# Performance work log

Hardware: AMD Instinct MI355X
Metric: run time of the kernel (lower is better)

## Reference

```python
import jax, jax.numpy as jnp
import numpy as np

T, B, I, H = 512, 64, 512, 512


def setup_inputs() -> dict:
    key = jax.random.key(0)
    k1, k2 = jax.random.split(key)
    x = jax.random.normal(k1, (T, B, I), dtype=jnp.float32)
    hidden_state = jnp.zeros((1, B, H), dtype=jnp.float32)
    cell_state = jnp.zeros((1, B, H), dtype=jnp.float32)
    # xavier-uniform-like init for weights, zeros for bias (matches init_weights)
    limit = float(np.sqrt(6.0 / ((I + H) + 4 * H)))
    W = jax.random.uniform(k2, (I + H, 4 * H), minval=-limit, maxval=limit, dtype=jnp.float32)
    b = jnp.zeros((4 * H,), dtype=jnp.float32)
    return {"x": x, "hidden_state": hidden_state, "cell_state": cell_state, "W": W, "b": b}


def reference(x, hidden_state, cell_state, W, b):
    # x: [T,B,I]; states: [1,B,H] -> squeeze leading dim for the scan carry
    h0 = hidden_state[0]
    c0 = cell_state[0]

    def step(carry, x_t):
        h, c = carry
        gates = jnp.concatenate([x_t, h], axis=-1) @ W + b  # [B,4H]
        f = jax.nn.sigmoid(gates[:, :H])
        i = jax.nn.sigmoid(gates[:, H:2 * H])
        cand = jnp.tanh(gates[:, 2 * H:3 * H])
        o = jax.nn.sigmoid(gates[:, 3 * H:])
        c_new = f * c + i * cand
        h_new = o * jnp.tanh(c_new)
        return (h_new, c_new), h_new

    (h_T, c_T), output = jax.lax.scan(step, (h0, c0), x)
    # hidden/cell states returned as [layers, B, H] with layers=1
    return output, (h_T[None], c_T[None])
```

## Files before the change

### kernel.cpp

```cpp
#include <hip/hip_runtime.h>
#include <cstdint>
#include <cstddef>

typedef unsigned short u16;
typedef unsigned long long u64;
typedef __attribute__((ext_vector_type(4))) float f32x4;
typedef __attribute__((ext_vector_type(8))) short s16x8;

#define T_STEPS 512
#define OUT_MAIN 16777216
#define HSLOT 65536

static __device__ __forceinline__ u16 f2bf(float f) {
  unsigned u = __builtin_bit_cast(unsigned, f);
  unsigned r = u + 0x7FFFu + ((u >> 16) & 1u);
  return (u16)(r >> 16);
}
static __device__ __forceinline__ float bf2f(u16 h) {
  unsigned u = ((unsigned)h) << 16;
  return __builtin_bit_cast(float, u);
}

__global__ void init_k(const float* __restrict__ W, const float* __restrict__ h0,
                       const float* __restrict__ c0,
                       u16* __restrict__ wthi, u16* __restrict__ wtlo,
                       u16* __restrict__ hbhi, u16* __restrict__ hblo,
                       float* __restrict__ cws, unsigned* __restrict__ flags) {
  const int NW = 1024 * 2048;
  const int NH = 64 * 512;
  const int total = NW + 2 * NH + 256;
  for (int idx = blockIdx.x * blockDim.x + threadIdx.x; idx < total;
       idx += gridDim.x * blockDim.x) {
    if (idx < NW) {
      int k = idx >> 11;
      int c = idx & 2047;
      float wv = W[idx];
      u16 hi = f2bf(wv);
      wthi[(size_t)c * 1024 + k] = hi;
      wtlo[(size_t)c * 1024 + k] = f2bf(wv - bf2f(hi));
    } else if (idx < NW + NH) {
      int r = idx - NW; int b = r >> 9; int k = r & 511;
      int g = b >> 3, rr = b & 7;
      float v = h0[r];
      u16 hi = f2bf(v);
      int pos = (g * 16 + rr) * 512 + k;
      hbhi[pos] = hi;
      hblo[pos] = f2bf(v - bf2f(hi));
    } else if (idx < NW + 2 * NH) {
      int r = idx - NW - NH;
      cws[r] = c0[r];
    } else {
      flags[idx - NW - 2 * NH] = 0u;
    }
  }
}

__global__ void convx_k(const float* __restrict__ x, u16* __restrict__ hi,
                        u16* __restrict__ lo, int n4) {
  for (int i = blockIdx.x * blockDim.x + threadIdx.x; i < n4;
       i += gridDim.x * blockDim.x) {
    float4 v = ((const float4*)x)[i];
    ushort4 h, l2;
    h.x = f2bf(v.x); l2.x = f2bf(v.x - bf2f(h.x));
    h.y = f2bf(v.y); l2.y = f2bf(v.y - bf2f(h.y));
    h.z = f2bf(v.z); l2.z = f2bf(v.z - bf2f(h.z));
    h.w = f2bf(v.w); l2.w = f2bf(v.w - bf2f(h.w));
    ((ushort4*)hi)[i] = h;
    ((ushort4*)lo)[i] = l2;
  }
}

__global__ void __launch_bounds__(256, 2)
gemm_k(const u16* __restrict__ xhi, const u16* __restrict__ xlo,
       const u16* __restrict__ wthi, const u16* __restrict__ wtlo,
       const float* __restrict__ bias, float* __restrict__ Gout) {
  __shared__ u16 Ah[4096], Al[4096], Bh[4096], Bl[4096];
  const int tid = threadIdx.x;
  const int nb = blockIdx.x & 15;
  const int mb = blockIdx.x >> 4;
  const int w = tid >> 6, l = tid & 63;
  const int wm = w >> 1, wn = w & 1;
  const int lr = l & 15, lq = l >> 4;

  const int pos0 = tid, pos1 = tid + 256;
  const int row0 = pos0 >> 2, row1 = pos1 >> 2;
  const int cc = (tid & 3) * 8;
  const size_t aOff0 = (size_t)(mb * 128 + row0) * 512 + cc;
  const size_t aOff1 = (size_t)(mb * 128 + row1) * 512 + cc;
  const size_t bOff0 = (size_t)(nb * 128 + row0) * 1024 + cc;
  const size_t bOff1 = (size_t)(nb * 128 + row1) * 1024 + cc;

  float bv[4];
  #pragma unroll
  for (int n = 0; n < 4; ++n) bv[n] = bias[nb * 128 + wn * 64 + n * 16 + lr];

  f32x4 acc[4][4] = {};
  s16x8 rA0, rA1, rAl0, rAl1, rB0, rB1, rBl0, rBl1;
  rA0  = *(const s16x8*)(xhi  + aOff0);
  rA1  = *(const s16x8*)(xhi  + aOff1);
  rAl0 = *(const s16x8*)(xlo  + aOff0);
  rAl1 = *(const s16x8*)(xlo  + aOff1);
  rB0  = *(const s16x8*)(wthi + bOff0);
  rB1  = *(const s16x8*)(wthi + bOff1);
  rBl0 = *(const s16x8*)(wtlo + bOff0);
  rBl1 = *(const s16x8*)(wtlo + bOff1);

  for (int kt = 0; kt < 16; ++kt) {
    *(s16x8*)&Ah[pos0 * 8] = rA0;  *(s16x8*)&Ah[pos1 * 8] = rA1;
    *(s16x8*)&Al[pos0 * 8] = rAl0; *(s16x8*)&Al[pos1 * 8] = rAl1;
    *(s16x8*)&Bh[pos0 * 8] = rB0;  *(s16x8*)&Bh[pos1 * 8] = rB1;
    *(s16x8*)&Bl[pos0 * 8] = rBl0; *(s16x8*)&Bl[pos1 * 8] = rBl1;
    __syncthreads();
    if (kt < 15) {
      const int k0 = (kt + 1) * 32;
      rA0  = *(const s16x8*)(xhi  + aOff0 + k0);
      rA1  = *(const s16x8*)(xhi  + aOff1 + k0);
      rAl0 = *(const s16x8*)(xlo  + aOff0 + k0);
      rAl1 = *(const s16x8*)(xlo  + aOff1 + k0);
      rB0  = *(const s16x8*)(wthi + bOff0 + k0);
      rB1  = *(const s16x8*)(wthi + bOff1 + k0);
      rBl0 = *(const s16x8*)(wtlo + bOff0 + k0);
      rBl1 = *(const s16x8*)(wtlo + bOff1 + k0);
    }
    s16x8 fAh[4], fAl[4], fBh[4], fBl[4];
    #pragma unroll
    for (int mm = 0; mm < 4; ++mm) {
      const int rrow = wm * 64 + mm * 16 + lr;
      fAh[mm] = *(const s16x8*)&Ah[rrow * 32 + lq * 8];
      fAl[mm] = *(const s16x8*)&Al[rrow * 32 + lq * 8];
    }
    #pragma unroll
    for (int nn = 0; nn < 4; ++nn) {
      const int crow = wn * 64 + nn * 16 + lr;
      fBh[nn] = *(const s16x8*)&Bh[crow * 32 + lq * 8];
      fBl[nn] = *(const s16x8*)&Bl[crow * 32 + lq * 8];
    }
    #pragma unroll
    for (int mm = 0; mm < 4; ++mm)
      #pragma unroll
      for (int nn = 0; nn < 4; ++nn) {
        acc[mm][nn] = __builtin_amdgcn_mfma_f32_16x16x32_bf16(fAh[mm], fBh[nn], acc[mm][nn], 0, 0, 0);
        acc[mm][nn] = __builtin_amdgcn_mfma_f32_16x16x32_bf16(fAh[mm], fBl[nn], acc[mm][nn], 0, 0, 0);
        acc[mm][nn] = __builtin_amdgcn_mfma_f32_16x16x32_bf16(fAl[mm], fBh[nn], acc[mm][nn], 0, 0, 0);
      }
    __syncthreads();
  }
  #pragma unroll
  for (int mm = 0; mm < 4; ++mm)
    #pragma unroll
    for (int nn = 0; nn < 4; ++nn)
      #pragma unroll
      for (int i = 0; i < 4; ++i) {
        const int row = mb * 128 + wm * 64 + mm * 16 + lq * 4 + i;
        const int col = nb * 128 + wn * 64 + nn * 16 + lr;
        Gout[(size_t)row * 2048 + col] = acc[mm][nn][i] + bv[nn];
      }
}

__global__ void __launch_bounds__(256, 1)
rec_k(const u16* __restrict__ wthi, const u16* __restrict__ wtlo,
      const float* __restrict__ Gbuf,
      u16* __restrict__ hbhi, u16* __restrict__ hblo,
      float* __restrict__ cws, float* __restrict__ out,
      unsigned* __restrict__ flags, int t0, int Tc) {
  const int g = blockIdx.x & 7;
  const int m = blockIdx.x >> 3;
  const int tid = threadIdx.x;
  const int w = tid >> 6;
  const int l = tid & 63;
  const int lr = l & 15, lq = l >> 4;

  __shared__ float part[4][8][64];

  s16x8 bhi[4][4], blo[4][4];
  #pragma unroll
  for (int nt = 0; nt < 4; ++nt) {
    const size_t cb = (size_t)(nt * 512 + m * 16 + lr) * 1024 + 512 + w * 128 + lq * 8;
    #pragma unroll
    for (int kt = 0; kt < 4; ++kt) {
      bhi[kt][nt] = *(const s16x8*)(wthi + cb + kt * 32);
      blo[kt][nt] = *(const s16x8*)(wtlo + cb + kt * 32);
    }
  }

  const int b0 = l >> 3;
  const int jj = (l & 7) * 2;
  float c0r = 0.f, c1r = 0.f;
  if (w == 0) {
    const float* cp = cws + (size_t)(g * 8 + b0) * 512 + m * 16 + jj;
    c0r = cp[0]; c1r = cp[1];
  }
  unsigned* gf = flags + g * 32;
  const int fragBase = (g * 16 + lr) * 128 + w * 32 + lq * 2;

  for (int tl = 0; tl < Tc; ++tl) {
    const int t = t0 + tl;
    float2 gv0, gv1, gv2, gv3;
    if (w == 0) {
      const float* gp = Gbuf + ((size_t)tl * 64 + g * 8 + b0) * 2048 + m * 16 + jj;
      gv0 = *(const float2*)(gp);
      gv1 = *(const float2*)(gp + 512);
      gv2 = *(const float2*)(gp + 1024);
      gv3 = *(const float2*)(gp + 1536);
      const unsigned tgt = (unsigned)t;
      int ok; unsigned spin = 0;
      do {
        unsigned v = 0xFFFFFFFFu;
        if (l < 32 && l != m)
          v = __hip_atomic_load(&gf[l], __ATOMIC_RELAXED, __HIP_MEMORY_SCOPE_AGENT);
        ok = __all((int)(v >= tgt));
        if (!ok) __builtin_amdgcn_s_sleep(2);
      } while (!ok && ++spin < (1u << 27));
    }
    __syncthreads();

    s16x8 ah[4], al[4];
    if (lr < 8) {
      const u64* sH = (const u64*)hbhi + (size_t)((t & 1) * (HSLOT / 4)) + fragBase;
      const u64* sL = (const u64*)hblo + (size_t)((t & 1) * (HSLOT / 4)) + fragBase;
      #pragma unroll
      for (int kt = 0; kt < 4; ++kt) {
        union { u64 q[2]; s16x8 v; } uh, ul;
        uh.q[0] = __hip_atomic_load((u64*)(sH + kt * 8),     __ATOMIC_RELAXED, __HIP_MEMORY_SCOPE_AGENT);
        uh.q[1] = __hip_atomic_load((u64*)(sH + kt * 8 + 1), __ATOMIC_RELAXED, __HIP_MEMORY_SCOPE_AGENT);
        ul.q[0] = __hip_atomic_load((u64*)(sL + kt * 8),     __ATOMIC_RELAXED, __HIP_MEMORY_SCOPE_AGENT);
        ul.q[1] = __hip_atomic_load((u64*)(sL + kt * 8 + 1), __ATOMIC_RELAXED, __HIP_MEMORY_SCOPE_AGENT);
        ah[kt] = uh.v; al[kt] = ul.v;
      }
    } else {
      #pragma unroll
      for (int kt = 0; kt < 4; ++kt) {
        ah[kt] = (s16x8)(short)0; al[kt] = (s16x8)(short)0;
      }
    }

    f32x4 acc[4] = {};
    #pragma unroll
    for (int kt = 0; kt < 4; ++kt)
      #pragma unroll
      for (int nt = 0; nt < 4; ++nt) {
        acc[nt] = __builtin_amdgcn_mfma_f32_16x16x32_bf16(ah[kt], bhi[kt][nt], acc[nt], 0, 0, 0);
        acc[nt] = __builtin_amdgcn_mfma_f32_16x16x32_bf16(ah[kt], blo[kt][nt], acc[nt], 0, 0, 0);
        acc[nt] = __builtin_amdgcn_mfma_f32_16x16x32_bf16(al[kt], bhi[kt][nt], acc[nt], 0, 0, 0);
      }
    if (l < 32) {
      #pragma unroll
      for (int nt = 0; nt < 4; ++nt)
        #pragma unroll
        for (int i = 0; i < 4; ++i)
          part[w][lq * 4 + i][nt * 16 + lr] = acc[nt][i];
    }
    __syncthreads();

    if (w == 0) {
      float ga[4][2];
      #pragma unroll
      for (int gi = 0; gi < 4; ++gi) {
        float2 s0 = *(const float2*)&part[0][b0][gi * 16 + jj];
        float2 s1 = *(const float2*)&part[1][b0][gi * 16 + jj];
        float2 s2 = *(const float2*)&part[2][b0][gi * 16 + jj];
        float2 s3 = *(const float2*)&part[3][b0][gi * 16 + jj];
        ga[gi][0] = (s0.x + s1.x) + (s2.x + s3.x);
        ga[gi][1] = (s0.y + s1.y) + (s2.y + s3.y);
      }
      float fg0 = ga[0][0] + gv0.x, fg1 = ga[0][1] + gv0.y;
      float ig0 = ga[1][0] + gv1.x, ig1 = ga[1][1] + gv1.y;
      float cg0 = ga[2][0] + gv2.x, cg1 = ga[2][1] + gv2.y;
      float og0 = ga[3][0] + gv3.x, og1 = ga[3][1] + gv3.y;
      float fs0 = 1.f / (1.f + __expf(-fg0)), fs1 = 1.f / (1.f + __expf(-fg1));
      float is0 = 1.f / (1.f + __expf(-ig0)), is1 = 1.f / (1.f + __expf(-ig1));
      float os0 = 1.f / (1.f + __expf(-og0)), os1 = 1.f / (1.f + __expf(-og1));
      float cd0 = tanhf(cg0), cd1 = tanhf(cg1);
      c0r = fs0 * c0r + is0 * cd0;
      c1r = fs1 * c1r + is1 * cd1;
      float hn0 = os0 * tanhf(c0r), hn1 = os1 * tanhf(c1r);
      u16 h0h = f2bf(hn0), h1h = f2bf(hn1);
      u16 l0h = f2bf(hn0 - bf2f(h0h)), l1h = f2bf(hn1 - bf2f(h1h));
      const int pdw = ((t + 1) & 1) * (HSLOT / 2) + (g * 16 + b0) * 256 + (m * 16 + jj) / 2;
      unsigned hw2 = (unsigned)h0h | ((unsigned)h1h << 16);
      unsigned lw2 = (unsigned)l0h | ((unsigned)l1h << 16);
      __hip_atomic_store((unsigned*)hbhi + pdw, hw2, __ATOMIC_RELAXED, __HIP_MEMORY_SCOPE_AGENT);
      __hip_atomic_store((unsigned*)hblo + pdw, lw2, __ATOMIC_RELAXED, __HIP_MEMORY_SCOPE_AGENT);
      asm volatile("s_waitcnt vmcnt(0)" ::: "memory");
      if (l == 0)
        __hip_atomic_store(&gf[m], (unsigned)(t + 1), __ATOMIC_RELAXED, __HIP_MEMORY_SCOPE_AGENT);
      float2 ho; ho.x = hn0; ho.y = hn1;
      *(float2*)(out + ((size_t)t * 64 + g * 8 + b0) * 512 + m * 16 + jj) = ho;
      if (t == T_STEPS - 1) {
        *(float2*)(out + (size_t)OUT_MAIN + (size_t)(g * 8 + b0) * 512 + m * 16 + jj) = ho;
        float2 co; co.x = c0r; co.y = c1r;
        *(float2*)(out + (size_t)OUT_MAIN + 32768 + (size_t)(g * 8 + b0) * 512 + m * 16 + jj) = co;
      }
      if (tl == Tc - 1) {
        float* cp = cws + (size_t)(g * 8 + b0) * 512 + m * 16 + jj;
        cp[0] = c0r; cp[1] = c1r;
      }
    }
  }
}

extern "C" void kernel_launch(void* const* d_in, const int* in_sizes, int n_in,
                              void* d_out, int out_size, void* d_ws, size_t ws_size,
                              hipStream_t stream) {
  const float* x  = (const float*)d_in[0];
  const float* h0 = (const float*)d_in[1];
  const float* c0 = (const float*)d_in[2];
  const float* W  = (const float*)d_in[3];
  const float* bs = (const float*)d_in[4];
  float* out = (float*)d_out;

  auto need = [](int tc) -> size_t {
    size_t s = 0;
    s += (size_t)tc * 524288;
    s += (size_t)tc * 131072;
    s += 2 * (size_t)4194304;
    s += 2 * (size_t)262144;
    s += 131072;
    s += 1024 + 8192;
    return s;
  };
  int Tc = 512;
  while (Tc > 2 && need(Tc) > ws_size) Tc >>= 1;

  char* p = (char*)d_ws;
  auto alloc = [&](size_t bytes) -> char* {
    char* r = p;
    p += (bytes + 255) & ~(size_t)255;
    return r;
  };
  float* Gbuf = (float*)alloc((size_t)Tc * 524288);
  u16* xhi  = (u16*)alloc((size_t)Tc * 65536);
  u16* xlo  = (u16*)alloc((size_t)Tc * 65536);
  u16* wthi = (u16*)alloc(4194304);
  u16* wtlo = (u16*)alloc(4194304);
  u16* hbhi = (u16*)alloc(262144);
  u16* hblo = (u16*)alloc(262144);
  float* cws = (float*)alloc(131072);
  unsigned* flags = (unsigned*)alloc(1024);

  hipLaunchKernelGGL(init_k, dim3(1024), dim3(256), 0, stream,
                     W, h0, c0, wthi, wtlo, hbhi, hblo, cws, flags);
  const int nch = 512 / Tc;
  for (int ck = 0; ck < nch; ++ck) {
    const float* xck = x + (size_t)ck * Tc * 64 * 512;
    int n4 = Tc * 64 * 512 / 4;
    hipLaunchKernelGGL(convx_k, dim3(1024), dim3(256), 0, stream, xck, xhi, xlo, n4);
    hipLaunchKernelGGL(gemm_k, dim3(Tc / 2 * 16), dim3(256), 0, stream,
                       xhi, xlo, wthi, wtlo, bs, Gbuf);
    hipLaunchKernelGGL(rec_k, dim3(256), dim3(256), 0, stream,
                       wthi, wtlo, Gbuf, hbhi, hblo, cws, out, flags, ck * Tc, Tc);
  }
}
```

Measured before the change: 2.272 ms.

## Replace flag-based step barrier with timestamp-tagged hidden state words

Removes the per-group flag array and the wait-for-flags-then-load sequence. Each hidden-state element becomes a 64-bit word that holds the step number alongside the bf16 hi/lo pair, so consumers spin directly on the data they need until every tag matches. This drops one global round trip, the store fence and the block barrier per timestep. It also spreads the gate epilogue over 32 lanes in each of the four waves instead of one wave, double-buffers the shared partial sums, and swaps tanhf for a clamped exp-based tanh. In exchange the hidden buffer doubles in size, each lane polls 32 words per spin, and the tanh approximation shifts numerics slightly.

Result: slower. 2.830 ms (+24.6%).

```diff
diff --git a/kernel.cpp b/kernel.cpp
--- a/kernel.cpp
+++ b/kernel.cpp
@@ -9,7 +9,7 @@
 
 #define T_STEPS 512
 #define OUT_MAIN 16777216
-#define HSLOT 65536
+#define HQSLOT 32768
 
 static __device__ __forceinline__ u16 f2bf(float f) {
   unsigned u = __builtin_bit_cast(unsigned, f);
@@ -24,11 +24,10 @@
 __global__ void init_k(const float* __restrict__ W, const float* __restrict__ h0,
                        const float* __restrict__ c0,
                        u16* __restrict__ wthi, u16* __restrict__ wtlo,
-                       u16* __restrict__ hbhi, u16* __restrict__ hblo,
-                       float* __restrict__ cws, unsigned* __restrict__ flags) {
+                       u64* __restrict__ hq, float* __restrict__ cws) {
   const int NW = 1024 * 2048;
   const int NH = 64 * 512;
-  const int total = NW + 2 * NH + 256;
+  const int total = NW + 2 * NH;
   for (int idx = blockIdx.x * blockDim.x + threadIdx.x; idx < total;
        idx += gridDim.x * blockDim.x) {
     if (idx < NW) {
@@ -39,18 +38,14 @@
       wthi[(size_t)c * 1024 + k] = hi;
       wtlo[(size_t)c * 1024 + k] = f2bf(wv - bf2f(hi));
     } else if (idx < NW + NH) {
-      int r = idx - NW; int b = r >> 9; int k = r & 511;
-      int g = b >> 3, rr = b & 7;
+      int r = idx - NW;
       float v = h0[r];
       u16 hi = f2bf(v);
-      int pos = (g * 16 + rr) * 512 + k;
-      hbhi[pos] = hi;
-      hblo[pos] = f2bf(v - bf2f(hi));
-    } else if (idx < NW + 2 * NH) {
+      u16 lo = f2bf(v - bf2f(hi));
+      hq[r] = ((u64)(unsigned)hi << 16) | (u64)(unsigned)lo;
+    } else {
       int r = idx - NW - NH;
       cws[r] = c0[r];
-    } else {
-      flags[idx - NW - 2 * NH] = 0u;
     }
   }
 }
@@ -159,10 +154,8 @@
 
 __global__ void __launch_bounds__(256, 1)
 rec_k(const u16* __restrict__ wthi, const u16* __restrict__ wtlo,
-      const float* __restrict__ Gbuf,
-      u16* __restrict__ hbhi, u16* __restrict__ hblo,
-      float* __restrict__ cws, float* __restrict__ out,
-      unsigned* __restrict__ flags, int t0, int Tc) {
+      const float* __restrict__ Gbuf, u64* __restrict__ hq,
+      float* __restrict__ cws, float* __restrict__ out, int t0, int Tc) {
   const int g = blockIdx.x & 7;
   const int m = blockIdx.x >> 3;
   const int tid = threadIdx.x;
@@ -170,7 +163,7 @@
   const int l = tid & 63;
   const int lr = l & 15, lq = l >> 4;
 
-  __shared__ float part[4][8][64];
+  __shared__ float part[2][4][8][64];
 
   s16x8 bhi[4][4], blo[4][4];
   #pragma unroll
@@ -183,50 +176,49 @@
     }
   }
 
-  const int b0 = l >> 3;
-  const int jj = (l & 7) * 2;
-  float c0r = 0.f, c1r = 0.f;
-  if (w == 0) {
-    const float* cp = cws + (size_t)(g * 8 + b0) * 512 + m * 16 + jj;
-    c0r = cp[0]; c1r = cp[1];
-  }
-  unsigned* gf = flags + g * 32;
-  const int fragBase = (g * 16 + lr) * 128 + w * 32 + lq * 2;
+  const int eb = 2 * w + (l >> 4);
+  const int eu = l & 15;
+  float cr = 0.f;
+  if (l < 32) cr = cws[(size_t)(g * 8 + eb) * 512 + m * 16 + eu];
+
+  const int rowBase = (g * 8 + lr) * 512 + w * 128 + lq * 8;
 
   for (int tl = 0; tl < Tc; ++tl) {
     const int t = t0 + tl;
-    float2 gv0, gv1, gv2, gv3;
-    if (w == 0) {
-      const float* gp = Gbuf + ((size_t)tl * 64 + g * 8 + b0) * 2048 + m * 16 + jj;
-      gv0 = *(const float2*)(gp);
-      gv1 = *(const float2*)(gp + 512);
-      gv2 = *(const float2*)(gp + 1024);
-      gv3 = *(const float2*)(gp + 1536);
-      const unsigned tgt = (unsigned)t;
-      int ok; unsigned spin = 0;
-      do {
-        unsigned v = 0xFFFFFFFFu;
-        if (l < 32 && l != m)
-          v = __hip_atomic_load(&gf[l], __ATOMIC_RELAXED, __HIP_MEMORY_SCOPE_AGENT);
-        ok = __all((int)(v >= tgt));
-        if (!ok) __builtin_amdgcn_s_sleep(2);
-      } while (!ok && ++spin < (1u << 27));
-    }
-    __syncthreads();
+    float gvf = 0.f, gvi = 0.f, gvc = 0.f, gvo = 0.f;
+    if (l < 32) {
+      const float* gp = Gbuf + ((size_t)tl * 64 + g * 8 + eb) * 2048 + m * 16 + eu;
+      gvf = gp[0]; gvi = gp[512]; gvc = gp[1024]; gvo = gp[1536];
+    }
+    const u64* hp = hq + (size_t)(t & 1) * HQSLOT + rowBase;
+    u64 q[4][8];
+    int ok; unsigned spin = 0;
+    do {
+      unsigned bad = 0;
+      if (lr < 8) {
+        #pragma unroll
+        for (int kt = 0; kt < 4; ++kt)
+          #pragma unroll
+          for (int j = 0; j < 8; ++j) {
+            q[kt][j] = __hip_atomic_load(hp + kt * 32 + j, __ATOMIC_RELAXED,
+                                         __HIP_MEMORY_SCOPE_AGENT);
+            bad |= (unsigned)(q[kt][j] >> 32) ^ (unsigned)t;
+          }
+      }
+      ok = __all(bad == 0);
+      if (!ok) __builtin_amdgcn_s_sleep(1);
+    } while (!ok && ++spin < (1u << 26));
 
     s16x8 ah[4], al[4];
     if (lr < 8) {
-      const u64* sH = (const u64*)hbhi + (size_t)((t & 1) * (HSLOT / 4)) + fragBase;
-      const u64* sL = (const u64*)hblo + (size_t)((t & 1) * (HSLOT / 4)) + fragBase;
-      #pragma unroll
-      for (int kt = 0; kt < 4; ++kt) {
-        union { u64 q[2]; s16x8 v; } uh, ul;
-        uh.q[0] = __hip_atomic_load((u64*)(sH + kt * 8),     __ATOMIC_RELAXED, __HIP_MEMORY_SCOPE_AGENT);
-        uh.q[1] = __hip_atomic_load((u64*)(sH + kt * 8 + 1), __ATOMIC_RELAXED, __HIP_MEMORY_SCOPE_AGENT);
-        ul.q[0] = __hip_atomic_load((u64*)(sL + kt * 8),     __ATOMIC_RELAXED, __HIP_MEMORY_SCOPE_AGENT);
-        ul.q[1] = __hip_atomic_load((u64*)(sL + kt * 8 + 1), __ATOMIC_RELAXED, __HIP_MEMORY_SCOPE_AGENT);
-        ah[kt] = uh.v; al[kt] = ul.v;
-      }
+      #pragma unroll
+      for (int kt = 0; kt < 4; ++kt)
+        #pragma unroll
+        for (int j = 0; j < 8; ++j) {
+          unsigned d = (unsigned)q[kt][j];
+          ah[kt][j] = (short)(d >> 16);
+          al[kt][j] = (short)(d & 0xFFFFu);
+        }
     } else {
       #pragma unroll
       for (int kt = 0; kt < 4; ++kt) {
@@ -243,58 +235,52 @@
         acc[nt] = __builtin_amdgcn_mfma_f32_16x16x32_bf16(ah[kt], blo[kt][nt], acc[nt], 0, 0, 0);
         acc[nt] = __builtin_amdgcn_mfma_f32_16x16x32_bf16(al[kt], bhi[kt][nt], acc[nt], 0, 0, 0);
       }
+    const int p = tl & 1;
     if (l < 32) {
       #pragma unroll
       for (int nt = 0; nt < 4; ++nt)
         #pragma unroll
         for (int i = 0; i < 4; ++i)
-          part[w][lq * 4 + i][nt * 16 + lr] = acc[nt][i];
+          part[p][w][lq * 4 + i][nt * 16 + lr] = acc[nt][i];
     }
     __syncthreads();
 
-    if (w == 0) {
-      float ga[4][2];
+    if (l < 32) {
+      float ga[4];
       #pragma unroll
       for (int gi = 0; gi < 4; ++gi) {
-        float2 s0 = *(const float2*)&part[0][b0][gi * 16 + jj];
-        float2 s1 = *(const float2*)&part[1][b0][gi * 16 + jj];
-        float2 s2 = *(const float2*)&part[2][b0][gi * 16 + jj];
-        float2 s3 = *(const float2*)&part[3][b0][gi * 16 + jj];
-        ga[gi][0] = (s0.x + s1.x) + (s2.x + s3.x);
-        ga[gi][1] = (s0.y + s1.y) + (s2.y + s3.y);
-      }
-      float fg0 = ga[0][0] + gv0.x, fg1 = ga[0][1] + gv0.y;
-      float ig0 = ga[1][0] + gv1.x, ig1 = ga[1][1] + gv1.y;
-      float cg0 = ga[2][0] + gv2.x, cg1 = ga[2][1] + gv2.y;
-      float og0 = ga[3][0] + gv3.x, og1 = ga[3][1] + gv3.y;
-      float fs0 = 1.f / (1.f + __expf(-fg0)), fs1 = 1.f / (1.f + __expf(-fg1));
-      float is0 = 1.f / (1.f + __expf(-ig0)), is1 = 1.f / (1.f + __expf(-ig1));
-      float os0 = 1.f / (1.f + __expf(-og0)), os1 = 1.f / (1.f + __expf(-og1));
-      float cd0 = tanhf(cg0), cd1 = tanhf(cg1);
-      c0r = fs0 * c0r + is0 * cd0;
-      c1r = fs1 * c1r + is1 * cd1;
-      float hn0 = os0 * tanhf(c0r), hn1 = os1 * tanhf(c1r);
-      u16 h0h = f2bf(hn0), h1h = f2bf(hn1);
-      u16 l0h = f2bf(hn0 - bf2f(h0h)), l1h = f2bf(hn1 - bf2f(h1h));
-      const int pdw = ((t + 1) & 1) * (HSLOT / 2) + (g * 16 + b0) * 256 + (m * 16 + jj) / 2;
-      unsigned hw2 = (unsigned)h0h | ((unsigned)h1h << 16);
-      unsigned lw2 = (unsigned)l0h | ((unsigned)l1h << 16);
-      __hip_atomic_store((unsigned*)hbhi + pdw, hw2, __ATOMIC_RELAXED, __HIP_MEMORY_SCOPE_AGENT);
-      __hip_atomic_store((unsigned*)hblo + pdw, lw2, __ATOMIC_RELAXED, __HIP_MEMORY_SCOPE_AGENT);
-      asm volatile("s_waitcnt vmcnt(0)" ::: "memory");
-      if (l == 0)
-        __hip_atomic_store(&gf[m], (unsigned)(t + 1), __ATOMIC_RELAXED, __HIP_MEMORY_SCOPE_AGENT);
-      float2 ho; ho.x = hn0; ho.y = hn1;
-      *(float2*)(out + ((size_t)t * 64 + g * 8 + b0) * 512 + m * 16 + jj) = ho;
+        float s0 = part[p][0][eb][gi * 16 + eu];
+        float s1 = part[p][1][eb][gi * 16 + eu];
+        float s2 = part[p][2][eb][gi * 16 + eu];
+        float s3 = part[p][3][eb][gi * 16 + eu];
+        ga[gi] = (s0 + s1) + (s2 + s3);
+      }
+      float fg = ga[0] + gvf, ig = ga[1] + gvi;
+      float cg = ga[2] + gvc, og = ga[3] + gvo;
+      float fs = 1.f / (1.f + __expf(-fg));
+      float is = 1.f / (1.f + __expf(-ig));
+      float os = 1.f / (1.f + __expf(-og));
+      float cgc = fminf(fmaxf(cg, -15.f), 15.f);
+      float e2c = __expf(2.f * cgc);
+      float cd = (e2c - 1.f) / (e2c + 1.f);
+      cr = fs * cr + is * cd;
+      float crc = fminf(fmaxf(cr, -15.f), 15.f);
+      float e2h = __expf(2.f * crc);
+      float th = (e2h - 1.f) / (e2h + 1.f);
+      float hn = os * th;
+      u16 hh = f2bf(hn);
+      u16 hl = f2bf(hn - bf2f(hh));
+      u64 qv = ((u64)(unsigned)(t + 1) << 32) | ((u64)(unsigned)hh << 16) | (u64)(unsigned)hl;
+      __hip_atomic_store(hq + (size_t)((t + 1) & 1) * HQSLOT +
+                             (size_t)(g * 8 + eb) * 512 + m * 16 + eu,
+                         qv, __ATOMIC_RELAXED, __HIP_MEMORY_SCOPE_AGENT);
+      out[((size_t)t * 64 + g * 8 + eb) * 512 + m * 16 + eu] = hn;
       if (t == T_STEPS - 1) {
-        *(float2*)(out + (size_t)OUT_MAIN + (size_t)(g * 8 + b0) * 512 + m * 16 + jj) = ho;
-        float2 co; co.x = c0r; co.y = c1r;
-        *(float2*)(out + (size_t)OUT_MAIN + 32768 + (size_t)(g * 8 + b0) * 512 + m * 16 + jj) = co;
-      }
-      if (tl == Tc - 1) {
-        float* cp = cws + (size_t)(g * 8 + b0) * 512 + m * 16 + jj;
-        cp[0] = c0r; cp[1] = c1r;
-      }
+        out[(size_t)OUT_MAIN + (size_t)(g * 8 + eb) * 512 + m * 16 + eu] = hn;
+        out[(size_t)OUT_MAIN + 32768 + (size_t)(g * 8 + eb) * 512 + m * 16 + eu] = cr;
+      }
+      if (tl == Tc - 1)
+        cws[(size_t)(g * 8 + eb) * 512 + m * 16 + eu] = cr;
     }
   }
 }
@@ -314,9 +300,9 @@
     s += (size_t)tc * 524288;
     s += (size_t)tc * 131072;
     s += 2 * (size_t)4194304;
-    s += 2 * (size_t)262144;
+    s += 524288;
     s += 131072;
-    s += 1024 + 8192;
+    s += 8192;
     return s;
   };
   int Tc = 512;
@@ -333,13 +319,11 @@
   u16* xlo  = (u16*)alloc((size_t)Tc * 65536);
   u16* wthi = (u16*)alloc(4194304);
   u16* wtlo = (u16*)alloc(4194304);
-  u16* hbhi = (u16*)alloc(262144);
-  u16* hblo = (u16*)alloc(262144);
+  u64* hq   = (u64*)alloc(524288);
   float* cws = (float*)alloc(131072);
-  unsigned* flags = (unsigned*)alloc(1024);
 
   hipLaunchKernelGGL(init_k, dim3(1024), dim3(256), 0, stream,
-                     W, h0, c0, wthi, wtlo, hbhi, hblo, cws, flags);
+                     W, h0, c0, wthi, wtlo, hq, cws);
   const int nch = 512 / Tc;
   for (int ck = 0; ck < nch; ++ck) {
     const float* xck = x + (size_t)ck * Tc * 64 * 512;
@@ -348,6 +332,6 @@
     hipLaunchKernelGGL(gemm_k, dim3(Tc / 2 * 16), dim3(256), 0, stream,
                        xhi, xlo, wthi, wtlo, bs, Gbuf);
     hipLaunchKernelGGL(rec_k, dim3(256), dim3(256), 0, stream,
-                       wthi, wtlo, Gbuf, hbhi, hblo, cws, out, flags, ck * Tc, Tc);
-  }
-}
+                       wthi, wtlo, Gbuf, hq, cws, out, ck * Tc, Tc);
+  }
+}
```
